# Kernel tuning notes

Hardware: AMD Instinct MI355X
Metric: run time of the kernel (lower is better)

Reference implementation:

```python
import jax, jax.numpy as jnp
import numpy as np

N, E, EV, D = 50000, 300000, 100000, 256
BN_EPS = 1e-5


def batchnorm(h, gamma, beta):
    # training-mode BN with batch statistics (biased var, matching torch normalization)
    mu = h.mean(axis=0)
    var = h.var(axis=0)
    return gamma * (h - mu) * jax.lax.rsqrt(var + BN_EPS) + beta


def mlp(h, W1, b1, g1, bt1, W2, b2):
    # Linear -> BN -> ReLU -> (Dropout=identity in eval) -> Linear
    h = h @ W1 + b1
    h = jax.nn.relu(batchnorm(h, g1, bt1))
    return h @ W2 + b2


def gine_conv(x, ei, ea, eps, W1, b1, g1, bt1, W2, b2):
    # message: ReLU(x_src + edge_attr); aggregate: scatter-add at dst; update: MLP((1+eps)*x + aggr)
    m = jax.nn.relu(x[ei[0]] + ea)                       # [E, D]
    aggr = jax.ops.segment_sum(m, ei[1], num_segments=N)  # [N, D]
    return mlp((1.0 + eps) * x + aggr, W1, b1, g1, bt1, W2, b2)


def setup_inputs() -> dict:
    key = jax.random.key(0)
    ks = jax.random.split(key, 16)
    s = 1.0 / np.sqrt(D)
    inp = {
        "x": jax.random.normal(ks[0], (N, D), jnp.float32),
        "edge_index": jax.random.randint(ks[1], (2, E), 0, N, jnp.int64),
        "edge_attr_emb": jax.random.normal(ks[2], (E, D), jnp.float32),
        "v_idx": jax.random.randint(ks[3], (2, EV), 0, N, jnp.int64),
        "v_edge_emb": jax.random.normal(ks[4], (EV, D), jnp.float32),
        # conv_down params
        "eps_down": jnp.zeros((), jnp.float32),
        "W1d": jax.random.normal(ks[5], (D, D), jnp.float32) * s,
        "b1d": jnp.zeros((D,), jnp.float32),
        "g1d": jnp.ones((D,), jnp.float32),
        "bt1d": jnp.zeros((D,), jnp.float32),
        "W2d": jax.random.normal(ks[6], (D, D), jnp.float32) * s,
        "b2d": jnp.zeros((D,), jnp.float32),
        # conv_up params
        "eps_up": jnp.zeros((), jnp.float32),
        "W1u": jax.random.normal(ks[7], (D, D), jnp.float32) * s,
        "b1u": jnp.zeros((D,), jnp.float32),
        "g1u": jnp.ones((D,), jnp.float32),
        "bt1u": jnp.zeros((D,), jnp.float32),
        "W2u": jax.random.normal(ks[8], (D, D), jnp.float32) * s,
        "b2u": jnp.zeros((D,), jnp.float32),
        # final BN + residual scales
        "bn_g": jnp.ones((D,), jnp.float32),
        "bn_b": jnp.zeros((D,), jnp.float32),
        "alpha1": jnp.asarray(1.0, jnp.float32),
        "alpha2": jnp.asarray(0.01, jnp.float32),
    }
    return inp


def reference(x, edge_index, edge_attr_emb, v_idx, v_edge_emb,
              eps_down, W1d, b1d, g1d, bt1d, W2d, b2d,
              eps_up, W1u, b1u, g1u, bt1u, W2u, b2u,
              bn_g, bn_b, alpha1, alpha2):
    h_down = gine_conv(x, edge_index, edge_attr_emb, eps_down, W1d, b1d, g1d, bt1d, W2d, b2d)
    h_up = gine_conv(x, v_idx, v_edge_emb, eps_up, W1u, b1u, g1u, bt1u, W2u, b2u)
    out = x + alpha1 * h_down + alpha2 * h_up
    return jax.nn.relu(batchnorm(out, bn_g, bn_b))
```

## Files before the change

kernel.cpp:

```cpp
#include <hip/hip_runtime.h>
#include <math.h>

#define N_NODES 50000
#define DIM 256
#define NE 300000
#define NEV 100000
#define BM 64
#define BK 64
#define NSLOT 8
#define GRID_PER ((N_NODES + BM - 1) / BM)

typedef float f32x4 __attribute__((ext_vector_type(4)));
typedef short s16x8 __attribute__((ext_vector_type(8)));

__device__ inline unsigned short f2bf(float f) {
    unsigned u = __float_as_uint(f);
    u += 0x7FFF + ((u >> 16) & 1);
    return (unsigned short)(u >> 16);
}
__device__ inline float bf2f(unsigned short s) {
    return __uint_as_float(((unsigned)s) << 16);
}
__device__ inline int swz(int row, int kg) {
    return row * BK + ((kg ^ (row & 7)) << 3);
}

__global__ __launch_bounds__(256) void prepw_kernel(
    const float* __restrict__ W1d, const float* __restrict__ W2d,
    const float* __restrict__ W1u, const float* __restrict__ W2u,
    unsigned short* __restrict__ Wt)
{
    int b = blockIdx.x;
    int w = b >> 8, n = b & 255, k = threadIdx.x;
    const float* W = (w == 0) ? W1d : (w == 1) ? W2d : (w == 2) ? W1u : W2u;
    Wt[(size_t)w * DIM * DIM + (size_t)n * DIM + k] = f2bf(W[(size_t)k * DIM + n]);
}

__global__ __launch_bounds__(256) void hist2_kernel(
    const int* __restrict__ ei, const int* __restrict__ vi,
    int* __restrict__ degD, int* __restrict__ degU)
{
    int i = blockIdx.x * blockDim.x + threadIdx.x;
    if (i < NE) atomicAdd(&degD[ei[NE + i]], 1);
    else if (i < NE + NEV) { int j = i - NE; atomicAdd(&degU[vi[NEV + j]], 1); }
}

__global__ __launch_bounds__(1024) void scan2_kernel(
    int* __restrict__ offD, int* __restrict__ curD,
    int* __restrict__ offU, int* __restrict__ curU)
{
    int* deg_offsets = (blockIdx.x == 0) ? offD : offU;
    int* cursor      = (blockIdx.x == 0) ? curD : curU;
    int E            = (blockIdx.x == 0) ? NE : NEV;
    __shared__ int part[1024];
    int t = threadIdx.x;
    const int CH = (N_NODES + 1023) / 1024;
    int beg = t * CH;
    int end = min(beg + CH, N_NODES);
    int s = 0;
    for (int i = beg; i < end; i++) s += deg_offsets[i];
    part[t] = s;
    __syncthreads();
    for (int off = 1; off < 1024; off <<= 1) {
        int v = part[t];
        int u = (t >= off) ? part[t - off] : 0;
        __syncthreads();
        part[t] = v + u;
        __syncthreads();
    }
    int run = (t > 0) ? part[t - 1] : 0;
    for (int i = beg; i < end; i++) {
        int dv = deg_offsets[i];
        deg_offsets[i] = run;
        cursor[i] = run;
        run += dv;
    }
    if (t == 1023) deg_offsets[N_NODES] = E;
}

__global__ __launch_bounds__(256) void fill2_kernel(
    const int* __restrict__ ei, const int* __restrict__ vi,
    int* __restrict__ curD, int* __restrict__ curU,
    int2* __restrict__ pairsD, int2* __restrict__ pairsU)
{
    int i = blockIdx.x * blockDim.x + threadIdx.x;
    if (i < NE) {
        int s = ei[i], d = ei[NE + i];
        int pos = atomicAdd(&curD[d], 1);
        pairsD[pos] = make_int2(i, s);
    } else if (i < NE + NEV) {
        int j = i - NE;
        int s = vi[j], d = vi[NEV + j];
        int pos = atomicAdd(&curU[d], 1);
        pairsU[pos] = make_int2(j, s);
    }
}

__device__ inline f32x4 ld4(const float* p) { return *(const f32x4*)p; }
__device__ inline f32x4 ldnt4(const float* p) {
    return __builtin_nontemporal_load((const f32x4*)p);
}
__device__ inline void acc_relu(f32x4& acc, f32x4 a, f32x4 b) {
    acc.x += fmaxf(a.x + b.x, 0.f);
    acc.y += fmaxf(a.y + b.y, 0.f);
    acc.z += fmaxf(a.z + b.z, 0.f);
    acc.w += fmaxf(a.w + b.w, 0.f);
}

__global__ __launch_bounds__(256) void gather2_kernel(
    const float* __restrict__ x, const float* __restrict__ ea,
    const float* __restrict__ vea,
    const int* __restrict__ offD, const int2* __restrict__ pairsD,
    const int* __restrict__ offU, const int2* __restrict__ pairsU,
    const float* __restrict__ epsd, const float* __restrict__ epsu,
    unsigned short* __restrict__ hD, unsigned short* __restrict__ hU)
{
    __shared__ f32x4 part[2][64];
    int warp = threadIdx.x >> 6;
    int lane = threadIdx.x & 63;
    int slotn = warp >> 1;
    int half = warp & 1;
    int nidx = blockIdx.x * 2 + slotn;
    bool down = nidx < N_NODES;
    int node = down ? nidx : nidx - N_NODES;
    const int* off      = down ? offD   : offU;
    const int2* pairs   = down ? pairsD : pairsU;
    const float* eat    = down ? ea     : vea;
    unsigned short* h   = down ? hD     : hU;
    float epsv = 1.0f + (down ? epsd[0] : epsu[0]);

    int beg = off[node], end = off[node + 1];
    f32x4 acc = {0.f, 0.f, 0.f, 0.f};
    int cofs = lane * 4;
    int p = beg + half;
    for (; p + 2 < end; p += 4) {
        int2 q0 = pairs[p], q1 = pairs[p + 2];
        f32x4 a0 = ld4(x + (size_t)q0.y * DIM + cofs);
        f32x4 b0 = ldnt4(eat + (size_t)q0.x * DIM + cofs);
        f32x4 a1 = ld4(x + (size_t)q1.y * DIM + cofs);
        f32x4 b1 = ldnt4(eat + (size_t)q1.x * DIM + cofs);
        acc_relu(acc, a0, b0);
        acc_relu(acc, a1, b1);
    }
    if (p < end) {
        int2 q0 = pairs[p];
        f32x4 a0 = ld4(x + (size_t)q0.y * DIM + cofs);
        f32x4 b0 = ldnt4(eat + (size_t)q0.x * DIM + cofs);
        acc_relu(acc, a0, b0);
    }
    if (half == 1) part[slotn][lane] = acc;
    __syncthreads();
    if (half == 0) {
        f32x4 o = part[slotn][lane];
        acc.x += o.x; acc.y += o.y; acc.z += o.z; acc.w += o.w;
        f32x4 xv = ld4(x + (size_t)node * DIM + cofs);
        acc.x = fmaf(epsv, xv.x, acc.x);
        acc.y = fmaf(epsv, xv.y, acc.y);
        acc.z = fmaf(epsv, xv.z, acc.z);
        acc.w = fmaf(epsv, xv.w, acc.w);
        ushort4 pk;
        pk.x = f2bf(acc.x); pk.y = f2bf(acc.y);
        pk.z = f2bf(acc.z); pk.w = f2bf(acc.w);
        *(ushort4*)(h + (size_t)node * DIM + cofs) = pk;
    }
}

__global__ __launch_bounds__(256) void scatter_kernel(
    const float* __restrict__ x, const float* __restrict__ ea,
    const int* __restrict__ idx, int E, float* __restrict__ buf)
{
    int wid = blockIdx.x * (blockDim.x >> 6) + (threadIdx.x >> 6);
    int lane = threadIdx.x & 63;
    if (wid >= E) return;
    int s = idx[wid];
    int d = idx[E + wid];
    float4 a = ((const float4*)(x + (size_t)s * DIM))[lane];
    float4 b = ((const float4*)(ea + (size_t)wid * DIM))[lane];
    float* dst = buf + (size_t)d * DIM + lane * 4;
    atomicAdd(dst + 0, fmaxf(a.x + b.x, 0.f));
    atomicAdd(dst + 1, fmaxf(a.y + b.y, 0.f));
    atomicAdd(dst + 2, fmaxf(a.z + b.z, 0.f));
    atomicAdd(dst + 3, fmaxf(a.w + b.w, 0.f));
}

__global__ __launch_bounds__(256) void conv_kernel(
    const float* __restrict__ x, const float* __restrict__ aggr,
    const float* __restrict__ eps_p, unsigned short* __restrict__ h)
{
    float epsv = 1.0f + eps_p[0];
    int i = blockIdx.x * blockDim.x + threadIdx.x;
    const int total = N_NODES * (DIM / 4);
    for (int f = i; f < total; f += gridDim.x * blockDim.x) {
        float4 xv = ((const float4*)x)[f];
        float4 av = ((const float4*)aggr)[f];
        ushort4 pk;
        pk.x = f2bf(fmaf(epsv, xv.x, av.x));
        pk.y = f2bf(fmaf(epsv, xv.y, av.y));
        pk.z = f2bf(fmaf(epsv, xv.z, av.z));
        pk.w = f2bf(fmaf(epsv, xv.w, av.w));
        ((ushort4*)h)[f] = pk;
    }
}

__global__ __launch_bounds__(256) void gemm1_both(
    const unsigned short* __restrict__ hD, const unsigned short* __restrict__ hU,
    const unsigned short* __restrict__ Wt1d, const unsigned short* __restrict__ Wt1u,
    const float* __restrict__ b1d, const float* __restrict__ b1u,
    unsigned short* __restrict__ t1D, unsigned short* __restrict__ t1U,
    float* __restrict__ sumD, float* __restrict__ sqD,
    float* __restrict__ sumU, float* __restrict__ sqU)
{
    __shared__ unsigned short As[BM * BK];
    __shared__ unsigned short Bs[DIM * BK];
    int blk = blockIdx.x;
    bool down = blk < GRID_PER;
    int bb = down ? blk : blk - GRID_PER;
    const unsigned short* h  = down ? hD   : hU;
    const unsigned short* Wt = down ? Wt1d : Wt1u;
    const float* bias        = down ? b1d  : b1u;
    unsigned short* t1       = down ? t1D  : t1U;
    float* ssum              = down ? sumD : sumU;
    float* ssq               = down ? sqD  : sqU;

    int t = threadIdx.x;
    int w = t >> 6, l = t & 63, lrow = l & 15, kgrp = l >> 4;
    int row0 = bb * BM;

    f32x4 acc[16];
    #pragma unroll
    for (int i = 0; i < 16; ++i) acc[i] = (f32x4){0.f, 0.f, 0.f, 0.f};

    for (int k0 = 0; k0 < DIM; k0 += BK) {
        __syncthreads();
        #pragma unroll
        for (int it = 0; it < 2; ++it) {
            int g = it * 256 + t, row = g >> 3, kg = g & 7;
            int gr = row0 + row;
            s16x8 v = {0, 0, 0, 0, 0, 0, 0, 0};
            if (gr < N_NODES)
                v = *(const s16x8*)&h[(size_t)gr * DIM + k0 + kg * 8];
            *(s16x8*)&As[swz(row, kg)] = v;
        }
        #pragma unroll
        for (int it = 0; it < 8; ++it) {
            int g = it * 256 + t, row = g >> 3, kg = g & 7;
            s16x8 v = *(const s16x8*)&Wt[(size_t)row * DIM + k0 + kg * 8];
            *(s16x8*)&Bs[swz(row, kg)] = v;
        }
        __syncthreads();
        #pragma unroll
        for (int kk = 0; kk < 2; ++kk) {
            s16x8 af[4], bf[4];
            #pragma unroll
            for (int mi = 0; mi < 4; ++mi)
                af[mi] = *(const s16x8*)&As[swz(mi * 16 + lrow, kk * 4 + kgrp)];
            #pragma unroll
            for (int ni = 0; ni < 4; ++ni)
                bf[ni] = *(const s16x8*)&Bs[swz(w * 64 + ni * 16 + lrow, kk * 4 + kgrp)];
            #pragma unroll
            for (int mi = 0; mi < 4; ++mi)
                #pragma unroll
                for (int ni = 0; ni < 4; ++ni)
                    acc[mi * 4 + ni] = __builtin_amdgcn_mfma_f32_16x16x32_bf16(
                        af[mi], bf[ni], acc[mi * 4 + ni], 0, 0, 0);
        }
    }
    int slot = bb & (NSLOT - 1);
    #pragma unroll
    for (int ni = 0; ni < 4; ++ni) {
        int col = w * 64 + ni * 16 + lrow;
        float bv = bias[col];
        float s = 0.f, q = 0.f;
        #pragma unroll
        for (int mi = 0; mi < 4; ++mi) {
            #pragma unroll
            for (int r = 0; r < 4; ++r) {
                int grow = row0 + mi * 16 + kgrp * 4 + r;
                if (grow < N_NODES) {
                    float v = acc[mi * 4 + ni][r] + bv;
                    t1[(size_t)grow * DIM + col] = f2bf(v);
                    s += v; q += v * v;
                }
            }
        }
        s += __shfl_xor(s, 16); q += __shfl_xor(q, 16);
        s += __shfl_xor(s, 32); q += __shfl_xor(q, 32);
        if (kgrp == 0) {
            atomicAdd(&ssum[slot * DIM + col], s);
            atomicAdd(&ssq[slot * DIM + col], q);
        }
    }
}

__global__ __launch_bounds__(256) void gemm2_both(
    const unsigned short* __restrict__ t1D, const unsigned short* __restrict__ t1U,
    const float* __restrict__ scD, const float* __restrict__ shD,
    const float* __restrict__ scU, const float* __restrict__ shU,
    const unsigned short* __restrict__ Wt2d, const unsigned short* __restrict__ Wt2u,
    const float* __restrict__ b2d, const float* __restrict__ b2u,
    const float* __restrict__ a1, const float* __restrict__ a2,
    float* __restrict__ C1, float* __restrict__ C2)
{
    __shared__ unsigned short As[BM * BK];
    __shared__ unsigned short Bs[DIM * BK];
    int blk = blockIdx.x;
    bool down = blk < GRID_PER;
    int bb = down ? blk : blk - GRID_PER;
    const unsigned short* t1 = down ? t1D  : t1U;
    const float* scale       = down ? scD  : scU;
    const float* shift       = down ? shD  : shU;
    const unsigned short* Wt = down ? Wt2d : Wt2u;
    const float* bias        = down ? b2d  : b2u;
    float alphav             = down ? a1[0] : a2[0];
    float* C                 = down ? C1   : C2;

    int t = threadIdx.x;
    int w = t >> 6, l = t & 63, lrow = l & 15, kgrp = l >> 4;
    int row0 = bb * BM;

    f32x4 acc[16];
    #pragma unroll
    for (int i = 0; i < 16; ++i) acc[i] = (f32x4){0.f, 0.f, 0.f, 0.f};

    for (int k0 = 0; k0 < DIM; k0 += BK) {
        __syncthreads();
        #pragma unroll
        for (int it = 0; it < 2; ++it) {
            int g = it * 256 + t, row = g >> 3, kg = g & 7;
            int gr = row0 + row;
            s16x8 pack = {0, 0, 0, 0, 0, 0, 0, 0};
            if (gr < N_NODES) {
                s16x8 tv = *(const s16x8*)(t1 + (size_t)gr * DIM + k0 + kg * 8);
                const float4* scp = (const float4*)(scale + k0 + kg * 8);
                const float4* shp = (const float4*)(shift + k0 + kg * 8);
                float4 s0 = scp[0], s1 = scp[1], h0 = shp[0], h1 = shp[1];
                pack[0] = f2bf(fmaxf(fmaf(bf2f((unsigned short)tv[0]), s0.x, h0.x), 0.f));
                pack[1] = f2bf(fmaxf(fmaf(bf2f((unsigned short)tv[1]), s0.y, h0.y), 0.f));
                pack[2] = f2bf(fmaxf(fmaf(bf2f((unsigned short)tv[2]), s0.z, h0.z), 0.f));
                pack[3] = f2bf(fmaxf(fmaf(bf2f((unsigned short)tv[3]), s0.w, h0.w), 0.f));
                pack[4] = f2bf(fmaxf(fmaf(bf2f((unsigned short)tv[4]), s1.x, h1.x), 0.f));
                pack[5] = f2bf(fmaxf(fmaf(bf2f((unsigned short)tv[5]), s1.y, h1.y), 0.f));
                pack[6] = f2bf(fmaxf(fmaf(bf2f((unsigned short)tv[6]), s1.z, h1.z), 0.f));
                pack[7] = f2bf(fmaxf(fmaf(bf2f((unsigned short)tv[7]), s1.w, h1.w), 0.f));
            }
            *(s16x8*)&As[swz(row, kg)] = pack;
        }
        #pragma unroll
        for (int it = 0; it < 8; ++it) {
            int g = it * 256 + t, row = g >> 3, kg = g & 7;
            s16x8 v = *(const s16x8*)&Wt[(size_t)row * DIM + k0 + kg * 8];
            *(s16x8*)&Bs[swz(row, kg)] = v;
        }
        __syncthreads();
        #pragma unroll
        for (int kk = 0; kk < 2; ++kk) {
            s16x8 af[4], bf[4];
            #pragma unroll
            for (int mi = 0; mi < 4; ++mi)
                af[mi] = *(const s16x8*)&As[swz(mi * 16 + lrow, kk * 4 + kgrp)];
            #pragma unroll
            for (int ni = 0; ni < 4; ++ni)
                bf[ni] = *(const s16x8*)&Bs[swz(w * 64 + ni * 16 + lrow, kk * 4 + kgrp)];
            #pragma unroll
            for (int mi = 0; mi < 4; ++mi)
                #pragma unroll
                for (int ni = 0; ni < 4; ++ni)
                    acc[mi * 4 + ni] = __builtin_amdgcn_mfma_f32_16x16x32_bf16(
                        af[mi], bf[ni], acc[mi * 4 + ni], 0, 0, 0);
        }
    }
    #pragma unroll
    for (int ni = 0; ni < 4; ++ni) {
        int col = w * 64 + ni * 16 + lrow;
        float bv = bias[col];
        #pragma unroll
        for (int mi = 0; mi < 4; ++mi) {
            #pragma unroll
            for (int r = 0; r < 4; ++r) {
                int grow = row0 + mi * 16 + kgrp * 4 + r;
                if (grow < N_NODES)
                    C[(size_t)grow * DIM + col] = alphav * (acc[mi * 4 + ni][r] + bv);
            }
        }
    }
}

__global__ __launch_bounds__(256) void combine_kernel(
    const float* __restrict__ x, const float* __restrict__ C1,
    const float* __restrict__ C2, float* __restrict__ out,
    float* __restrict__ ssum, float* __restrict__ ssq)
{
    __shared__ f32x4 sS[4][64];
    __shared__ f32x4 sQ[4][64];
    int t = threadIdx.x;
    int cq = t & 63, rg = t >> 6;
    f32x4 s = {0.f, 0.f, 0.f, 0.f}, q = {0.f, 0.f, 0.f, 0.f};
    const int rowstep = gridDim.x * 4;
    for (int row = blockIdx.x * 4 + rg; row < N_NODES; row += rowstep) {
        size_t f = (size_t)row * 64 + cq;
        f32x4 v = ((const f32x4*)x)[f] + ((const f32x4*)C1)[f] + ((const f32x4*)C2)[f];
        ((f32x4*)out)[f] = v;
        s += v; q += v * v;
    }
    sS[rg][cq] = s; sQ[rg][cq] = q;
    __syncthreads();
    if (rg == 0) {
        s = sS[0][cq] + sS[1][cq] + sS[2][cq] + sS[3][cq];
        q = sQ[0][cq] + sQ[1][cq] + sQ[2][cq] + sQ[3][cq];
        int slot = blockIdx.x & (NSLOT - 1);
        int c = cq * 4;
        atomicAdd(&ssum[slot * DIM + c + 0], s.x);
        atomicAdd(&ssum[slot * DIM + c + 1], s.y);
        atomicAdd(&ssum[slot * DIM + c + 2], s.z);
        atomicAdd(&ssum[slot * DIM + c + 3], s.w);
        atomicAdd(&ssq[slot * DIM + c + 0], q.x);
        atomicAdd(&ssq[slot * DIM + c + 1], q.y);
        atomicAdd(&ssq[slot * DIM + c + 2], q.z);
        atomicAdd(&ssq[slot * DIM + c + 3], q.w);
    }
}

__device__ inline void bn_finalize(
    const float* ssum, const float* ssq, const float* g, const float* b,
    float* scale, float* shift, int c)
{
    float s = 0.f, q = 0.f;
    #pragma unroll
    for (int k = 0; k < NSLOT; ++k) { s += ssum[k * DIM + c]; q += ssq[k * DIM + c]; }
    const float invN = 1.0f / (float)N_NODES;
    float mu = s * invN;
    float var = q * invN - mu * mu;
    float sc = g[c] * rsqrtf(var + 1e-5f);
    scale[c] = sc;
    shift[c] = b[c] - mu * sc;
}

__global__ void finalize2_kernel(
    const float* __restrict__ sumD, const float* __restrict__ sqD,
    const float* __restrict__ g1d, const float* __restrict__ bt1d,
    float* __restrict__ scD, float* __restrict__ shD,
    const float* __restrict__ sumU, const float* __restrict__ sqU,
    const float* __restrict__ g1u, const float* __restrict__ bt1u,
    float* __restrict__ scU, float* __restrict__ shU)
{
    int t = threadIdx.x;
    int c = t & (DIM - 1);
    if (t < DIM) bn_finalize(sumD, sqD, g1d, bt1d, scD, shD, c);
    else         bn_finalize(sumU, sqU, g1u, bt1u, scU, shU, c);
}

__global__ void finalize_kernel(
    const float* __restrict__ ssum, const float* __restrict__ ssq,
    const float* __restrict__ g, const float* __restrict__ b,
    float* __restrict__ scale, float* __restrict__ shift)
{
    bn_finalize(ssum, ssq, g, b, scale, shift, threadIdx.x);
}

__global__ __launch_bounds__(256) void bnrelu_kernel(
    float* __restrict__ out, const float* __restrict__ scale,
    const float* __restrict__ shift)
{
    int idx = blockIdx.x * blockDim.x + threadIdx.x;
    const int total = N_NODES * (DIM / 4);
    for (int f = idx; f < total; f += gridDim.x * blockDim.x) {
        float4 v = ((float4*)out)[f];
        int c = (f * 4) & (DIM - 1);
        float4 sc = *(const float4*)(scale + c);
        float4 sh = *(const float4*)(shift + c);
        v.x = fmaxf(v.x * sc.x + sh.x, 0.0f);
        v.y = fmaxf(v.y * sc.y + sh.y, 0.0f);
        v.z = fmaxf(v.z * sc.z + sh.z, 0.0f);
        v.w = fmaxf(v.w * sc.w + sh.w, 0.0f);
        ((float4*)out)[f] = v;
    }
}

extern "C" void kernel_launch(void* const* d_in, const int* in_sizes, int n_in,
                              void* d_out, int out_size, void* d_ws, size_t ws_size,
                              hipStream_t stream)
{
    const float* x    = (const float*)d_in[0];
    const int*   ei   = (const int*)  d_in[1];
    const float* ea   = (const float*)d_in[2];
    const int*   vi   = (const int*)  d_in[3];
    const float* vea  = (const float*)d_in[4];
    const float* epsd = (const float*)d_in[5];
    const float* W1d  = (const float*)d_in[6];
    const float* b1d  = (const float*)d_in[7];
    const float* g1d  = (const float*)d_in[8];
    const float* bt1d = (const float*)d_in[9];
    const float* W2d  = (const float*)d_in[10];
    const float* b2d  = (const float*)d_in[11];
    const float* epsu = (const float*)d_in[12];
    const float* W1u  = (const float*)d_in[13];
    const float* b1u  = (const float*)d_in[14];
    const float* g1u  = (const float*)d_in[15];
    const float* bt1u = (const float*)d_in[16];
    const float* W2u  = (const float*)d_in[17];
    const float* b2u  = (const float*)d_in[18];
    const float* bng  = (const float*)d_in[19];
    const float* bnb  = (const float*)d_in[20];
    const float* a1   = (const float*)d_in[21];
    const float* a2   = (const float*)d_in[22];

    float* out = (float*)d_out;

    char* p = (char*)d_ws;
    unsigned short* hD  = (unsigned short*)p;  p += (size_t)N_NODES * DIM * 2;
    unsigned short* hU  = (unsigned short*)p;  p += (size_t)N_NODES * DIM * 2;
    unsigned short* t1D = (unsigned short*)p;  p += (size_t)N_NODES * DIM * 2;
    unsigned short* t1U = (unsigned short*)p;  p += (size_t)N_NODES * DIM * 2;
    unsigned short* Wt  = (unsigned short*)p;  p += (size_t)4 * DIM * DIM * 2;
    float* C1 = (float*)p;                     p += (size_t)N_NODES * DIM * 4;
    float* C2 = (float*)p;                     p += (size_t)N_NODES * DIM * 4;
    float* scD = (float*)p;                    p += DIM * 4;
    float* shD = (float*)p;                    p += DIM * 4;
    float* scU = (float*)p;                    p += DIM * 4;
    float* shU = (float*)p;                    p += DIM * 4;
    char* zero_base = p;
    float* stats = (float*)p;                  p += (size_t)6 * NSLOT * DIM * 4;
    int* offD = (int*)p;                       p += (size_t)(N_NODES + 1) * 4;
    int* offU = (int*)p;                       p += (size_t)(N_NODES + 1) * 4;
    size_t zero_bytes = (size_t)(p - zero_base);
    int* curD = (int*)p;                       p += (size_t)N_NODES * 4;
    int* curU = (int*)p;                       p += (size_t)N_NODES * 4;
    char* union_base = p;
    int2* pairsD = (int2*)p;                   p += (size_t)NE * 8;
    int2* pairsU = (int2*)p;                   p += (size_t)NEV * 8;
    size_t need_csr = (size_t)(p - (char*)d_ws);
    float* aggr = (float*)union_base;
    size_t need_fb = (size_t)(union_base - (char*)d_ws) + (size_t)N_NODES * DIM * 4;
    bool use_csr = ws_size >= need_csr;

    float* sumD = stats;
    float* sqD  = stats + 1 * NSLOT * DIM;
    float* sumU = stats + 2 * NSLOT * DIM;
    float* sqU  = stats + 3 * NSLOT * DIM;
    float* sumF = stats + 4 * NSLOT * DIM;
    float* sqF  = stats + 5 * NSLOT * DIM;

    unsigned short* Wt1d = Wt;
    unsigned short* Wt2d = Wt + 1 * (size_t)DIM * DIM;
    unsigned short* Wt1u = Wt + 2 * (size_t)DIM * DIM;
    unsigned short* Wt2u = Wt + 3 * (size_t)DIM * DIM;

    hipMemsetAsync(zero_base, 0, zero_bytes, stream);
    prepw_kernel<<<4 * DIM, 256, 0, stream>>>(W1d, W2d, W1u, W2u, Wt);

    if (use_csr) {
        hist2_kernel<<<(NE + NEV + 255) / 256, 256, 0, stream>>>(ei, vi, offD, offU);
        scan2_kernel<<<2, 1024, 0, stream>>>(offD, curD, offU, curU);
        fill2_kernel<<<(NE + NEV + 255) / 256, 256, 0, stream>>>(
            ei, vi, curD, curU, pairsD, pairsU);
        gather2_kernel<<<N_NODES, 256, 0, stream>>>(
            x, ea, vea, offD, pairsD, offU, pairsU, epsd, epsu, hD, hU);
    } else if (ws_size >= need_fb) {
        hipMemsetAsync(aggr, 0, (size_t)N_NODES * DIM * 4, stream);
        scatter_kernel<<<(NE + 3) / 4, 256, 0, stream>>>(x, ea, ei, NE, aggr);
        conv_kernel<<<2048, 256, 0, stream>>>(x, aggr, epsd, hD);
        hipMemsetAsync(aggr, 0, (size_t)N_NODES * DIM * 4, stream);
        scatter_kernel<<<(NEV + 3) / 4, 256, 0, stream>>>(x, vea, vi, NEV, aggr);
        conv_kernel<<<2048, 256, 0, stream>>>(x, aggr, epsu, hU);
    }

    gemm1_both<<<2 * GRID_PER, 256, 0, stream>>>(
        hD, hU, Wt1d, Wt1u, b1d, b1u, t1D, t1U, sumD, sqD, sumU, sqU);
    finalize2_kernel<<<1, 2 * DIM, 0, stream>>>(
        sumD, sqD, g1d, bt1d, scD, shD, sumU, sqU, g1u, bt1u, scU, shU);

    gemm2_both<<<2 * GRID_PER, 256, 0, stream>>>(
        t1D, t1U, scD, shD, scU, shU, Wt2d, Wt2u, b2d, b2u, a1, a2, C1, C2);

    combine_kernel<<<1024, 256, 0, stream>>>(x, C1, C2, out, sumF, sqF);
    finalize_kernel<<<1, 256, 0, stream>>>(sumF, sqF, bng, bnb, scD, shD);
    bnrelu_kernel<<<2048, 256, 0, stream>>>(out, scD, shD);
}
```

Before: 487.2 us.

## Fuse second GEMMs, residual combine, and BN finalize into one kernel

Each block now computes both the down and up second-layer GEMMs for its row tile in sequence. It adds x and accumulates the final BN statistics directly in the epilogue, so the C1/C2 fp32 intermediates and the separate combine kernel go away. The per-layer BN finalization moves into the GEMM prologue, and the final one into bnrelu_kernel, which drops two single-block launches. In exchange the kernel holds two accumulator sets, which raises register pressure, and the grid is half as large with longer per-block work.

```diff
diff --git a/kernel.cpp b/kernel.cpp
--- a/kernel.cpp
+++ b/kernel.cpp
@@ -292,134 +292,6 @@
     }
 }
 
-__global__ __launch_bounds__(256) void gemm2_both(
-    const unsigned short* __restrict__ t1D, const unsigned short* __restrict__ t1U,
-    const float* __restrict__ scD, const float* __restrict__ shD,
-    const float* __restrict__ scU, const float* __restrict__ shU,
-    const unsigned short* __restrict__ Wt2d, const unsigned short* __restrict__ Wt2u,
-    const float* __restrict__ b2d, const float* __restrict__ b2u,
-    const float* __restrict__ a1, const float* __restrict__ a2,
-    float* __restrict__ C1, float* __restrict__ C2)
-{
-    __shared__ unsigned short As[BM * BK];
-    __shared__ unsigned short Bs[DIM * BK];
-    int blk = blockIdx.x;
-    bool down = blk < GRID_PER;
-    int bb = down ? blk : blk - GRID_PER;
-    const unsigned short* t1 = down ? t1D  : t1U;
-    const float* scale       = down ? scD  : scU;
-    const float* shift       = down ? shD  : shU;
-    const unsigned short* Wt = down ? Wt2d : Wt2u;
-    const float* bias        = down ? b2d  : b2u;
-    float alphav             = down ? a1[0] : a2[0];
-    float* C                 = down ? C1   : C2;
-
-    int t = threadIdx.x;
-    int w = t >> 6, l = t & 63, lrow = l & 15, kgrp = l >> 4;
-    int row0 = bb * BM;
-
-    f32x4 acc[16];
-    #pragma unroll
-    for (int i = 0; i < 16; ++i) acc[i] = (f32x4){0.f, 0.f, 0.f, 0.f};
-
-    for (int k0 = 0; k0 < DIM; k0 += BK) {
-        __syncthreads();
-        #pragma unroll
-        for (int it = 0; it < 2; ++it) {
-            int g = it * 256 + t, row = g >> 3, kg = g & 7;
-            int gr = row0 + row;
-            s16x8 pack = {0, 0, 0, 0, 0, 0, 0, 0};
-            if (gr < N_NODES) {
-                s16x8 tv = *(const s16x8*)(t1 + (size_t)gr * DIM + k0 + kg * 8);
-                const float4* scp = (const float4*)(scale + k0 + kg * 8);
-                const float4* shp = (const float4*)(shift + k0 + kg * 8);
-                float4 s0 = scp[0], s1 = scp[1], h0 = shp[0], h1 = shp[1];
-                pack[0] = f2bf(fmaxf(fmaf(bf2f((unsigned short)tv[0]), s0.x, h0.x), 0.f));
-                pack[1] = f2bf(fmaxf(fmaf(bf2f((unsigned short)tv[1]), s0.y, h0.y), 0.f));
-                pack[2] = f2bf(fmaxf(fmaf(bf2f((unsigned short)tv[2]), s0.z, h0.z), 0.f));
-                pack[3] = f2bf(fmaxf(fmaf(bf2f((unsigned short)tv[3]), s0.w, h0.w), 0.f));
-                pack[4] = f2bf(fmaxf(fmaf(bf2f((unsigned short)tv[4]), s1.x, h1.x), 0.f));
-                pack[5] = f2bf(fmaxf(fmaf(bf2f((unsigned short)tv[5]), s1.y, h1.y), 0.f));
-                pack[6] = f2bf(fmaxf(fmaf(bf2f((unsigned short)tv[6]), s1.z, h1.z), 0.f));
-                pack[7] = f2bf(fmaxf(fmaf(bf2f((unsigned short)tv[7]), s1.w, h1.w), 0.f));
-            }
-            *(s16x8*)&As[swz(row, kg)] = pack;
-        }
-        #pragma unroll
-        for (int it = 0; it < 8; ++it) {
-            int g = it * 256 + t, row = g >> 3, kg = g & 7;
-            s16x8 v = *(const s16x8*)&Wt[(size_t)row * DIM + k0 + kg * 8];
-            *(s16x8*)&Bs[swz(row, kg)] = v;
-        }
-        __syncthreads();
-        #pragma unroll
-        for (int kk = 0; kk < 2; ++kk) {
-            s16x8 af[4], bf[4];
-            #pragma unroll
-            for (int mi = 0; mi < 4; ++mi)
-                af[mi] = *(const s16x8*)&As[swz(mi * 16 + lrow, kk * 4 + kgrp)];
-            #pragma unroll
-            for (int ni = 0; ni < 4; ++ni)
-                bf[ni] = *(const s16x8*)&Bs[swz(w * 64 + ni * 16 + lrow, kk * 4 + kgrp)];
-            #pragma unroll
-            for (int mi = 0; mi < 4; ++mi)
-                #pragma unroll
-                for (int ni = 0; ni < 4; ++ni)
-                    acc[mi * 4 + ni] = __builtin_amdgcn_mfma_f32_16x16x32_bf16(
-                        af[mi], bf[ni], acc[mi * 4 + ni], 0, 0, 0);
-        }
-    }
-    #pragma unroll
-    for (int ni = 0; ni < 4; ++ni) {
-        int col = w * 64 + ni * 16 + lrow;
-        float bv = bias[col];
-        #pragma unroll
-        for (int mi = 0; mi < 4; ++mi) {
-            #pragma unroll
-            for (int r = 0; r < 4; ++r) {
-                int grow = row0 + mi * 16 + kgrp * 4 + r;
-                if (grow < N_NODES)
-                    C[(size_t)grow * DIM + col] = alphav * (acc[mi * 4 + ni][r] + bv);
-            }
-        }
-    }
-}
-
-__global__ __launch_bounds__(256) void combine_kernel(
-    const float* __restrict__ x, const float* __restrict__ C1,
-    const float* __restrict__ C2, float* __restrict__ out,
-    float* __restrict__ ssum, float* __restrict__ ssq)
-{
-    __shared__ f32x4 sS[4][64];
-    __shared__ f32x4 sQ[4][64];
-    int t = threadIdx.x;
-    int cq = t & 63, rg = t >> 6;
-    f32x4 s = {0.f, 0.f, 0.f, 0.f}, q = {0.f, 0.f, 0.f, 0.f};
-    const int rowstep = gridDim.x * 4;
-    for (int row = blockIdx.x * 4 + rg; row < N_NODES; row += rowstep) {
-        size_t f = (size_t)row * 64 + cq;
-        f32x4 v = ((const f32x4*)x)[f] + ((const f32x4*)C1)[f] + ((const f32x4*)C2)[f];
-        ((f32x4*)out)[f] = v;
-        s += v; q += v * v;
-    }
-    sS[rg][cq] = s; sQ[rg][cq] = q;
-    __syncthreads();
-    if (rg == 0) {
-        s = sS[0][cq] + sS[1][cq] + sS[2][cq] + sS[3][cq];
-        q = sQ[0][cq] + sQ[1][cq] + sQ[2][cq] + sQ[3][cq];
-        int slot = blockIdx.x & (NSLOT - 1);
-        int c = cq * 4;
-        atomicAdd(&ssum[slot * DIM + c + 0], s.x);
-        atomicAdd(&ssum[slot * DIM + c + 1], s.y);
-        atomicAdd(&ssum[slot * DIM + c + 2], s.z);
-        atomicAdd(&ssum[slot * DIM + c + 3], s.w);
-        atomicAdd(&ssq[slot * DIM + c + 0], q.x);
-        atomicAdd(&ssq[slot * DIM + c + 1], q.y);
-        atomicAdd(&ssq[slot * DIM + c + 2], q.z);
-        atomicAdd(&ssq[slot * DIM + c + 3], q.w);
-    }
-}
-
 __device__ inline void bn_finalize(
     const float* ssum, const float* ssq, const float* g, const float* b,
     float* scale, float* shift, int c)
@@ -435,39 +307,173 @@
     shift[c] = b[c] - mu * sc;
 }
 
-__global__ void finalize2_kernel(
+__global__ __launch_bounds__(256) void gemm2_fused(
+    const unsigned short* __restrict__ t1D, const unsigned short* __restrict__ t1U,
     const float* __restrict__ sumD, const float* __restrict__ sqD,
     const float* __restrict__ g1d, const float* __restrict__ bt1d,
-    float* __restrict__ scD, float* __restrict__ shD,
     const float* __restrict__ sumU, const float* __restrict__ sqU,
     const float* __restrict__ g1u, const float* __restrict__ bt1u,
-    float* __restrict__ scU, float* __restrict__ shU)
-{
+    const unsigned short* __restrict__ Wt2d, const unsigned short* __restrict__ Wt2u,
+    const float* __restrict__ b2d, const float* __restrict__ b2u,
+    const float* __restrict__ a1, const float* __restrict__ a2,
+    const float* __restrict__ x, float* __restrict__ out,
+    float* __restrict__ sumF, float* __restrict__ sqF)
+{
+    __shared__ unsigned short As[BM * BK];
+    __shared__ unsigned short Bs[DIM * BK];
+    __shared__ float scDl[DIM], shDl[DIM], scUl[DIM], shUl[DIM];
     int t = threadIdx.x;
-    int c = t & (DIM - 1);
-    if (t < DIM) bn_finalize(sumD, sqD, g1d, bt1d, scD, shD, c);
-    else         bn_finalize(sumU, sqU, g1u, bt1u, scU, shU, c);
-}
-
-__global__ void finalize_kernel(
-    const float* __restrict__ ssum, const float* __restrict__ ssq,
-    const float* __restrict__ g, const float* __restrict__ b,
-    float* __restrict__ scale, float* __restrict__ shift)
-{
-    bn_finalize(ssum, ssq, g, b, scale, shift, threadIdx.x);
+    int w = t >> 6, l = t & 63, lrow = l & 15, kgrp = l >> 4;
+    int bb = blockIdx.x;
+    int row0 = bb * BM;
+
+    bn_finalize(sumD, sqD, g1d, bt1d, scDl, shDl, t);
+    bn_finalize(sumU, sqU, g1u, bt1u, scUl, shUl, t);
+    float a1v = a1[0], a2v = a2[0];
+
+    f32x4 acc[16], accO[16];
+    #pragma unroll
+    for (int i = 0; i < 16; ++i) acc[i] = (f32x4){0.f, 0.f, 0.f, 0.f};
+
+    for (int k0 = 0; k0 < DIM; k0 += BK) {
+        __syncthreads();
+        #pragma unroll
+        for (int it = 0; it < 2; ++it) {
+            int g = it * 256 + t, row = g >> 3, kg = g & 7;
+            int gr = row0 + row;
+            s16x8 pack = {0, 0, 0, 0, 0, 0, 0, 0};
+            if (gr < N_NODES) {
+                s16x8 tv = *(const s16x8*)(t1D + (size_t)gr * DIM + k0 + kg * 8);
+                #pragma unroll
+                for (int j = 0; j < 8; ++j) {
+                    int c = k0 + kg * 8 + j;
+                    pack[j] = f2bf(fmaxf(fmaf(bf2f((unsigned short)tv[j]), scDl[c], shDl[c]), 0.f));
+                }
+            }
+            *(s16x8*)&As[swz(row, kg)] = pack;
+        }
+        #pragma unroll
+        for (int it = 0; it < 8; ++it) {
+            int g = it * 256 + t, row = g >> 3, kg = g & 7;
+            s16x8 v = *(const s16x8*)&Wt2d[(size_t)row * DIM + k0 + kg * 8];
+            *(s16x8*)&Bs[swz(row, kg)] = v;
+        }
+        __syncthreads();
+        #pragma unroll
+        for (int kk = 0; kk < 2; ++kk) {
+            s16x8 af[4], bf[4];
+            #pragma unroll
+            for (int mi = 0; mi < 4; ++mi)
+                af[mi] = *(const s16x8*)&As[swz(mi * 16 + lrow, kk * 4 + kgrp)];
+            #pragma unroll
+            for (int ni = 0; ni < 4; ++ni)
+                bf[ni] = *(const s16x8*)&Bs[swz(w * 64 + ni * 16 + lrow, kk * 4 + kgrp)];
+            #pragma unroll
+            for (int mi = 0; mi < 4; ++mi)
+                #pragma unroll
+                for (int ni = 0; ni < 4; ++ni)
+                    acc[mi * 4 + ni] = __builtin_amdgcn_mfma_f32_16x16x32_bf16(
+                        af[mi], bf[ni], acc[mi * 4 + ni], 0, 0, 0);
+        }
+    }
+    #pragma unroll
+    for (int ni = 0; ni < 4; ++ni) {
+        float bv = b2d[w * 64 + ni * 16 + lrow];
+        #pragma unroll
+        for (int mi = 0; mi < 4; ++mi) {
+            #pragma unroll
+            for (int r = 0; r < 4; ++r)
+                accO[mi * 4 + ni][r] = a1v * (acc[mi * 4 + ni][r] + bv);
+            acc[mi * 4 + ni] = (f32x4){0.f, 0.f, 0.f, 0.f};
+        }
+    }
+
+    for (int k0 = 0; k0 < DIM; k0 += BK) {
+        __syncthreads();
+        #pragma unroll
+        for (int it = 0; it < 2; ++it) {
+            int g = it * 256 + t, row = g >> 3, kg = g & 7;
+            int gr = row0 + row;
+            s16x8 pack = {0, 0, 0, 0, 0, 0, 0, 0};
+            if (gr < N_NODES) {
+                s16x8 tv = *(const s16x8*)(t1U + (size_t)gr * DIM + k0 + kg * 8);
+                #pragma unroll
+                for (int j = 0; j < 8; ++j) {
+                    int c = k0 + kg * 8 + j;
+                    pack[j] = f2bf(fmaxf(fmaf(bf2f((unsigned short)tv[j]), scUl[c], shUl[c]), 0.f));
+                }
+            }
+            *(s16x8*)&As[swz(row, kg)] = pack;
+        }
+        #pragma unroll
+        for (int it = 0; it < 8; ++it) {
+            int g = it * 256 + t, row = g >> 3, kg = g & 7;
+            s16x8 v = *(const s16x8*)&Wt2u[(size_t)row * DIM + k0 + kg * 8];
+            *(s16x8*)&Bs[swz(row, kg)] = v;
+        }
+        __syncthreads();
+        #pragma unroll
+        for (int kk = 0; kk < 2; ++kk) {
+            s16x8 af[4], bf[4];
+            #pragma unroll
+            for (int mi = 0; mi < 4; ++mi)
+                af[mi] = *(const s16x8*)&As[swz(mi * 16 + lrow, kk * 4 + kgrp)];
+            #pragma unroll
+            for (int ni = 0; ni < 4; ++ni)
+                bf[ni] = *(const s16x8*)&Bs[swz(w * 64 + ni * 16 + lrow, kk * 4 + kgrp)];
+            #pragma unroll
+            for (int mi = 0; mi < 4; ++mi)
+                #pragma unroll
+                for (int ni = 0; ni < 4; ++ni)
+                    acc[mi * 4 + ni] = __builtin_amdgcn_mfma_f32_16x16x32_bf16(
+                        af[mi], bf[ni], acc[mi * 4 + ni], 0, 0, 0);
+        }
+    }
+
+    int slot = bb & (NSLOT - 1);
+    #pragma unroll
+    for (int ni = 0; ni < 4; ++ni) {
+        int col = w * 64 + ni * 16 + lrow;
+        float bvU = b2u[col];
+        float s = 0.f, q = 0.f;
+        #pragma unroll
+        for (int mi = 0; mi < 4; ++mi) {
+            #pragma unroll
+            for (int r = 0; r < 4; ++r) {
+                int grow = row0 + mi * 16 + kgrp * 4 + r;
+                if (grow < N_NODES) {
+                    size_t o = (size_t)grow * DIM + col;
+                    float v = x[o] + accO[mi * 4 + ni][r]
+                            + a2v * (acc[mi * 4 + ni][r] + bvU);
+                    out[o] = v;
+                    s += v; q += v * v;
+                }
+            }
+        }
+        s += __shfl_xor(s, 16); q += __shfl_xor(q, 16);
+        s += __shfl_xor(s, 32); q += __shfl_xor(q, 32);
+        if (kgrp == 0) {
+            atomicAdd(&sumF[slot * DIM + col], s);
+            atomicAdd(&sqF[slot * DIM + col], q);
+        }
+    }
 }
 
 __global__ __launch_bounds__(256) void bnrelu_kernel(
-    float* __restrict__ out, const float* __restrict__ scale,
-    const float* __restrict__ shift)
-{
+    float* __restrict__ out,
+    const float* __restrict__ sumF, const float* __restrict__ sqF,
+    const float* __restrict__ bng, const float* __restrict__ bnb)
+{
+    __shared__ float scl[DIM], shl[DIM];
+    bn_finalize(sumF, sqF, bng, bnb, scl, shl, threadIdx.x);
+    __syncthreads();
     int idx = blockIdx.x * blockDim.x + threadIdx.x;
     const int total = N_NODES * (DIM / 4);
     for (int f = idx; f < total; f += gridDim.x * blockDim.x) {
         float4 v = ((float4*)out)[f];
         int c = (f * 4) & (DIM - 1);
-        float4 sc = *(const float4*)(scale + c);
-        float4 sh = *(const float4*)(shift + c);
+        float4 sc = *(const float4*)(scl + c);
+        float4 sh = *(const float4*)(shl + c);
         v.x = fmaxf(v.x * sc.x + sh.x, 0.0f);
         v.y = fmaxf(v.y * sc.y + sh.y, 0.0f);
         v.z = fmaxf(v.z * sc.z + sh.z, 0.0f);
@@ -512,12 +518,6 @@
     unsigned short* t1D = (unsigned short*)p;  p += (size_t)N_NODES * DIM * 2;
     unsigned short* t1U = (unsigned short*)p;  p += (size_t)N_NODES * DIM * 2;
     unsigned short* Wt  = (unsigned short*)p;  p += (size_t)4 * DIM * DIM * 2;
-    float* C1 = (float*)p;                     p += (size_t)N_NODES * DIM * 4;
-    float* C2 = (float*)p;                     p += (size_t)N_NODES * DIM * 4;
-    float* scD = (float*)p;                    p += DIM * 4;
-    float* shD = (float*)p;                    p += DIM * 4;
-    float* scU = (float*)p;                    p += DIM * 4;
-    float* shU = (float*)p;                    p += DIM * 4;
     char* zero_base = p;
     float* stats = (float*)p;                  p += (size_t)6 * NSLOT * DIM * 4;
     int* offD = (int*)p;                       p += (size_t)(N_NODES + 1) * 4;
@@ -566,13 +566,10 @@
 
     gemm1_both<<<2 * GRID_PER, 256, 0, stream>>>(
         hD, hU, Wt1d, Wt1u, b1d, b1u, t1D, t1U, sumD, sqD, sumU, sqU);
-    finalize2_kernel<<<1, 2 * DIM, 0, stream>>>(
-        sumD, sqD, g1d, bt1d, scD, shD, sumU, sqU, g1u, bt1u, scU, shU);
-
-    gemm2_both<<<2 * GRID_PER, 256, 0, stream>>>(
-        t1D, t1U, scD, shD, scU, shU, Wt2d, Wt2u, b2d, b2u, a1, a2, C1, C2);
-
-    combine_kernel<<<1024, 256, 0, stream>>>(x, C1, C2, out, sumF, sqF);
-    finalize_kernel<<<1, 256, 0, stream>>>(sumF, sqF, bng, bnb, scD, shD);
-    bnrelu_kernel<<<2048, 256, 0, stream>>>(out, scD, shD);
-}
+
+    gemm2_fused<<<GRID_PER, 256, 0, stream>>>(
+        t1D, t1U, sumD, sqD, g1d, bt1d, sumU, sqU, g1u, bt1u,
+        Wt2d, Wt2u, b2d, b2u, a1, a2, x, out, sumF, sqF);
+
+    bnrelu_kernel<<<2048, 256, 0, stream>>>(out, sumF, sqF, bng, bnb);
+}
```

Measured after the change: 438.4 us. 1.11x faster.
